# Kernel optimization log

Measured on AMD Instinct MI355X. Metric: run time of the kernel, lower is better.

Reference implementation:

```python
import jax, jax.numpy as jnp
import numpy as np

NEG = -1e30  # finite stand-in for -inf (grad-safe)


def _ctc_loss(logits, logit_length, labels):
    """CTC negative log-likelihood per example.

    logits: [B, T, V] (blank index 0), logit_length: [B] int,
    labels: [B, L] int padded with -1.
    """
    B, T, V = logits.shape
    L = labels.shape[1]
    S = 2 * L + 1  # extended label length (blanks interleaved)

    label_len = jnp.sum(labels >= 0, axis=1)          # [B]
    lab = jnp.where(labels < 0, 0, labels)            # pad -> blank for safe gathers
    ext = jnp.zeros((B, S), dtype=lab.dtype).at[:, 1::2].set(lab)  # [B, S]

    log_probs = jax.nn.log_softmax(logits, axis=-1)   # [B, T, V]
    # emission log-prob of each extended symbol at each time: [B, T, S]
    lp_ext = jnp.take_along_axis(log_probs, ext[:, None, :], axis=2)

    # skip (s-2) transition allowed only for non-blank symbols differing from s-2
    ext_m2 = jnp.pad(ext, ((0, 0), (2, 0)), constant_values=-1)[:, :S]
    allow_skip = (ext != 0) & (ext != ext_m2)         # [B, S]

    alpha0 = (jnp.full((B, S), NEG, dtype=logits.dtype)
              .at[:, 0].set(lp_ext[:, 0, 0])
              .at[:, 1].set(lp_ext[:, 0, 1]))

    def step(alpha, lp_t):  # alpha, lp_t: [B, S]
        a1 = jnp.pad(alpha, ((0, 0), (1, 0)), constant_values=NEG)[:, :S]
        a2 = jnp.pad(alpha, ((0, 0), (2, 0)), constant_values=NEG)[:, :S]
        a2 = jnp.where(allow_skip, a2, NEG)
        new = lp_t + jnp.logaddexp(jnp.logaddexp(alpha, a1), a2)
        return new, new

    lp_tm = jnp.moveaxis(lp_ext, 1, 0)                # [T, B, S] time-major
    _, alphas = jax.lax.scan(step, alpha0, lp_tm[1:])
    alphas = jnp.concatenate([alpha0[None], alphas], axis=0)  # [T, B, S]

    # read trellis at each example's final frame
    t_idx = jnp.clip(logit_length, 1, T) - 1          # [B]
    alpha_fin = alphas[t_idx, jnp.arange(B)]          # [B, S]
    s_last = 2 * label_len                            # final blank position
    a_blank = jnp.take_along_axis(alpha_fin, s_last[:, None], axis=1)[:, 0]
    a_label = jnp.take_along_axis(alpha_fin, jnp.maximum(s_last - 1, 0)[:, None], axis=1)[:, 0]
    return -jnp.logaddexp(a_blank, a_label)           # [B]


def setup_inputs() -> dict:
    key = jax.random.key(0)
    k1, k2, k3, k4 = jax.random.split(key, 4)
    B, T, V, L = 64, 1000, 64, 150
    logits = jax.random.normal(k1, (B, T, V), dtype=jnp.float32)
    # raw sample counts; min 100000 guarantees logit_length >= 2*L+1 (valid CTC)
    audio_length = jax.random.randint(k2, (B,), 100000, 256000, dtype=jnp.int32)
    label_vals = jax.random.randint(k3, (B, L), 1, V, dtype=jnp.int32)  # no blanks
    label_len = jax.random.randint(k4, (B,), 100, L + 1, dtype=jnp.int32)
    pos = jnp.arange(L)[None, :]
    labels = jnp.where(pos < label_len[:, None], label_vals, -1)
    return {"logits": logits, "audio_length": audio_length, "labels": labels}


def reference(logits, audio_length, labels):
    # length transform from train_step: ceil((len+1)/128), then truncating /2
    ll = jnp.ceil((audio_length.astype(jnp.float32) + 1.0) / 128.0).astype(jnp.int32)
    logit_length = ll // 2
    per_ex = _ctc_loss(logits, logit_length, labels)
    return jnp.mean(per_ex)
```

## Files before the change

kernel.cpp:

```cpp
#include <hip/hip_runtime.h>


#define VV 64
#define L2E 1.4426950408889634f
#define LN2D 0.6931471805599453
#define CH 8

__global__ __launch_bounds__(256) void lse_kernel(const float4* __restrict__ lg4,
                                                  const int* __restrict__ audio_len,
                                                  double* __restrict__ sumlse,
                                                  float* __restrict__ out,
                                                  int T) {
    if (blockIdx.x == 0 && blockIdx.y == 0 && threadIdx.x == 0) out[0] = 0.0f;
    const int b = blockIdx.y;
    const int tl = threadIdx.x >> 4;
    const int q = threadIdx.x & 15;
    const int t = blockIdx.x * 16 + tl;
    int al = audio_len[b];
    int Tb = ((al + 128) >> 7) >> 1;
    if (Tb < 1) Tb = 1;
    if (Tb > T) Tb = T;

    __shared__ double part[16];
    double v = 0.0;
    if (t < Tb) {
        float4 x = lg4[((size_t)b * T + t) * 16 + q];
        float m = fmaxf(fmaxf(x.x, x.y), fmaxf(x.z, x.w));
        #pragma unroll
        for (int off = 8; off >= 1; off >>= 1) m = fmaxf(m, __shfl_xor(m, off));
        float s = __expf(x.x - m) + __expf(x.y - m) + __expf(x.z - m) + __expf(x.w - m);
        #pragma unroll
        for (int off = 8; off >= 1; off >>= 1) s += __shfl_xor(s, off);
        v = (double)(m + __logf(s));
    }
    if (q == 0) part[tl] = v;
    __syncthreads();
    if (threadIdx.x == 0) {
        double s = 0.0;
        #pragma unroll
        for (int i = 0; i < 16; ++i) s += part[i];
        if (s != 0.0) atomicAdd(&sumlse[b], s);
    }
}


#define LOADM(E, TB, DIRSGN)                                                    \
    do {                                                                        \
        _Pragma("unroll")                                                       \
        for (int k_ = 0; k_ < CH; ++k_) {                                       \
            int tt_ = (TB) + (DIRSGN) * k_;                                     \
            if (tt_ < 0) tt_ = 0;                                               \
            if (tt_ > tf) tt_ = tf;                                             \
            const float* fr_ = lg + ((size_t)tt_ << 6);                         \
            _Pragma("unroll")                                                   \
            for (int i_ = 0; i_ < 5; ++i_) E[i_][k_] = fr_[sym[i_]];            \
        }                                                                       \
    } while (0)

#define CONV(E)                                                                 \
    do {                                                                        \
        _Pragma("unroll")                                                       \
        for (int i_ = 0; i_ < 5; ++i_) {                                        \
            _Pragma("unroll")                                                   \
            for (int k_ = 0; k_ < CH; ++k_)                                     \
                E[i_][k_] = __builtin_amdgcn_exp2f(E[i_][k_] * L2E);            \
        }                                                                       \
    } while (0)

#define PROCF(E, STEP0, MASKED)                                                 \
    do {                                                                        \
        _Pragma("unroll")                                                       \
        for (int k_ = 0; k_ < CH; ++k_) {                                       \
            double a_ = __shfl_up(p[4], 1);                                     \
            double b_ = __shfl_up(p[3], 1);                                     \
            if (lane == 0) { a_ = 0.0; b_ = 0.0; }                              \
            double e_[5];                                                       \
            _Pragma("unroll")                                                   \
            for (int i_ = 0; i_ < 5; ++i_) e_[i_] = (double)E[i_][k_];          \
            double n0_ = e_[0] * (p[0] + a_ + skd[0] * b_);                     \
            double n1_ = e_[1] * (p[1] + p[0] + skd[1] * a_);                   \
            double n2_ = e_[2] * (p[2] + p[1] + skd[2] * p[0]);                 \
            double n3_ = e_[3] * (p[3] + p[2] + skd[3] * p[1]);                 \
            double n4_ = e_[4] * (p[4] + p[3] + skd[4] * p[2]);                 \
            if (MASKED) {                                                       \
                bool act_ = ((STEP0) + k_) < nst_;                              \
                p[0] = act_ ? n0_ : p[0]; p[1] = act_ ? n1_ : p[1];             \
                p[2] = act_ ? n2_ : p[2]; p[3] = act_ ? n3_ : p[3];             \
                p[4] = act_ ? n4_ : p[4];                                       \
            } else {                                                            \
                p[0] = n0_; p[1] = n1_; p[2] = n2_; p[3] = n3_; p[4] = n4_;     \
            }                                                                   \
        }                                                                       \
    } while (0)

#define PROCB(E, STEP0, MASKED)                                                 \
    do {                                                                        \
        _Pragma("unroll")                                                       \
        for (int k_ = 0; k_ < CH; ++k_) {                                       \
               \
            double pn0_ = __shfl_down(p[0], 1);                                 \
            double pn1_ = __shfl_down(p[1], 1);                                 \
            float en0_ = __shfl_down(E[0][k_], 1);                              \
            float en1_ = __shfl_down(E[1][k_], 1);                              \
            if (lane == 63) { pn0_ = 0.0; pn1_ = 0.0; }                         \
            double u_[5];                                                       \
            _Pragma("unroll")                                                   \
            for (int i_ = 0; i_ < 5; ++i_) u_[i_] = p[i_] * (double)E[i_][k_];  \
            double u5_ = pn0_ * (double)en0_;                                   \
            double u6_ = pn1_ * (double)en1_;                                   \
            double n0_ = u_[0] + u_[1] + skd[2] * u_[2];                        \
            double n1_ = u_[1] + u_[2] + skd[3] * u_[3];                        \
            double n2_ = u_[2] + u_[3] + skd[4] * u_[4];                        \
            double n3_ = u_[3] + u_[4] + skd[5] * u5_;                          \
            double n4_ = u_[4] + u5_ + skd[6] * u6_;                            \
            if (MASKED) {                                                       \
                bool act_ = ((STEP0) + k_) < nst_;                              \
                p[0] = act_ ? n0_ : p[0]; p[1] = act_ ? n1_ : p[1];             \
                p[2] = act_ ? n2_ : p[2]; p[3] = act_ ? n3_ : p[3];             \
                p[4] = act_ ? n4_ : p[4];                                       \
            } else {                                                            \
                p[0] = n0_; p[1] = n1_; p[2] = n2_; p[3] = n3_; p[4] = n4_;     \
            }                                                                   \
        }                                                                       \
    } while (0)

#define RENORM()                                                                \
    do {                                                                        \
        double mx_ = fmax(fmax(fmax(p[0], p[1]), fmax(p[2], p[3])), p[4]);      \
        int ex_ = (__double2hiint(mx_) >> 20) & 0x7ff;                          \
        _Pragma("unroll")                                                       \
        for (int o_ = 32; o_ >= 1; o_ >>= 1) {                                  \
            int t_ = __shfl_xor(ex_, o_);                                       \
            ex_ = t_ > ex_ ? t_ : ex_;                                          \
        }                                                                       \
        if (ex_ > 0) {                                                          \
            Cexp += ex_ - 1023;                                                 \
            double r_ = __hiloint2double((2046 - ex_) << 20, 0);                \
            _Pragma("unroll")                                                   \
            for (int i_ = 0; i_ < 5; ++i_) p[i_] *= r_;                         \
        }                                                                       \
    } while (0)

__global__ __launch_bounds__(128, 1) void ctc_kernel(const float* __restrict__ lgall,
                                                     const int* __restrict__ audio_len,
                                                     const int* __restrict__ labels,
                                                     const double* __restrict__ sumlse,
                                                     float* __restrict__ out,
                                                     int B, int T, int L) {
    const int b = blockIdx.x;
    const int tid = threadIdx.x;
    const int lane = tid & 63;
    const int wid = tid >> 6;
    const int S = 2 * L + 1;
    const float* lg = lgall + (size_t)b * T * VV;

    int al = audio_len[b];
    int Tb = ((al + 128) >> 7) >> 1;
    if (Tb < 1) Tb = 1;
    if (Tb > T) Tb = T;
    const int tf = Tb - 1;
    const int mid = tf >> 1;

    __shared__ int lab_sh[152];
    __shared__ double beta_sh[324];
    __shared__ double sumlse_sh;
    __shared__ int cexpb_sh;

    for (int k = tid; k < L; k += 128) lab_sh[k] = labels[b * L + k];
    __syncthreads();

    int cnt = 0;
    for (int k = lane; k < L; k += 64) cnt += (lab_sh[k] >= 0) ? 1 : 0;
    #pragma unroll
    for (int off = 32; off >= 1; off >>= 1) cnt += __shfl_xor(cnt, off);
    const int s_last = 2 * cnt;

    int sym[5];
    double skd[7];
    #pragma unroll
    for (int i = 0; i < 7; ++i) {
        int s = lane * 5 + i;
        int sy = 0;
        double sk = 0.0;
        if (s < S && (s & 1)) {
            int lv = lab_sh[s >> 1];
            sy = lv < 0 ? 0 : lv;
            if (s >= 3 && sy != 0) {
                int lv2 = lab_sh[(s >> 1) - 1];
                int s2 = lv2 < 0 ? 0 : lv2;
                sk = (sy != s2) ? 1.0 : 0.0;
            }
        }
        if (i < 5) sym[i] = sy;
        skd[i] = sk;
    }

    double p[5];
    int Cexp = 0;

    if (wid == 0) {
        {
            #pragma unroll
            for (int i = 0; i < 5; ++i) {
                float x = lg[sym[i]];
                int s = lane * 5 + i;
                p[i] = (s <= 1) ? (double)__builtin_amdgcn_exp2f(x * L2E) : 0.0;
            }
        }
        const int nst_ = mid;
        if (nst_ > 0) {
            const int nch = (nst_ + CH - 1) / CH;
            float eA[5][CH], eB[5][CH];
            LOADM(eA, 1, +1);
            int base = 1, c = 0, step0 = 0;
            for (;;) {
                if (c + 1 < nch) LOADM(eB, base + CH, +1);
                CONV(eA);
                if (c == nch - 1) { PROCF(eA, step0, 1); break; }
                PROCF(eA, step0, 0);
                ++c; step0 += CH; base += CH;
                if ((c & 3) == 0) RENORM();
                if (c + 1 < nch) LOADM(eA, base + CH, +1);
                CONV(eB);
                if (c == nch - 1) { PROCF(eB, step0, 1); break; }
                PROCF(eB, step0, 0);
                ++c; step0 += CH; base += CH;
                if ((c & 3) == 0) RENORM();
            }
        }
        RENORM();
    } else {
        #pragma unroll
        for (int i = 0; i < 5; ++i) {
            int s = lane * 5 + i;
            p[i] = (s == s_last || s == s_last - 1) ? 1.0 : 0.0;
        }
        const int nst_ = tf - mid;
        if (nst_ > 0) {
            const int nch = (nst_ + CH - 1) / CH;
            float eA[5][CH], eB[5][CH];
            LOADM(eA, tf, -1);
            int base = tf, c = 0, step0 = 0;
            for (;;) {
                if (c + 1 < nch) LOADM(eB, base - CH, -1);
                CONV(eA);
                if (c == nch - 1) { PROCB(eA, step0, 1); break; }
                PROCB(eA, step0, 0);
                ++c; step0 += CH; base -= CH;
                if ((c & 3) == 0) RENORM();
                if (c + 1 < nch) LOADM(eA, base - CH, -1);
                CONV(eB);
                if (c == nch - 1) { PROCB(eB, step0, 1); break; }
                PROCB(eB, step0, 0);
                ++c; step0 += CH; base -= CH;
                if ((c & 3) == 0) RENORM();
            }
        }
        RENORM();
        #pragma unroll
        for (int i = 0; i < 5; ++i) beta_sh[lane * 5 + i] = p[i];
        if (lane == 0) { cexpb_sh = Cexp; sumlse_sh = sumlse[b]; }
    }
    __syncthreads();

    if (wid == 0) {
        double dot = 0.0;
        #pragma unroll
        for (int i = 0; i < 5; ++i) dot += p[i] * beta_sh[lane * 5 + i];
        #pragma unroll
        for (int o = 32; o >= 1; o >>= 1) dot += __shfl_xor(dot, o);
        if (lane == 0) {
            dot = fmax(dot, 1e-290);
            double lp = log(dot) + (double)(Cexp + cexpb_sh) * LN2D - sumlse_sh;
            atomicAdd(out, (float)(-lp / (double)B));
        }
    }
}

extern "C" void kernel_launch(void* const* d_in, const int* in_sizes, int n_in,
                              void* d_out, int out_size, void* d_ws, size_t ws_size,
                              hipStream_t stream) {
    const float* logits = (const float*)d_in[0];
    const int* audio = (const int*)d_in[1];
    const int* labels = (const int*)d_in[2];
    float* out = (float*)d_out;

    int B = in_sizes[1];
    int L = in_sizes[2] / B;
    int T = in_sizes[0] / (B * VV);

    double* sumlse = (double*)d_ws;
    hipMemsetAsync(sumlse, 0, (size_t)B * sizeof(double), stream);

    dim3 gA((T + 15) / 16, B);
    lse_kernel<<<gA, 256, 0, stream>>>((const float4*)logits, audio, sumlse, out, T);
    ctc_kernel<<<B, 128, 0, stream>>>(logits, audio, labels, sumlse, out, B, T, L);
}
```

Baseline: 169.8 us.

## Fuse log-sum-exp into CTC kernel via third wave and hand-scheduled loads

```diff
diff --git a/kernel.cpp b/kernel.cpp
--- a/kernel.cpp
+++ b/kernel.cpp
@@ -6,56 +6,44 @@
 #define LN2D 0.6931471805599453
 #define CH 8
 
-__global__ __launch_bounds__(256) void lse_kernel(const float4* __restrict__ lg4,
-                                                  const int* __restrict__ audio_len,
-                                                  double* __restrict__ sumlse,
-                                                  float* __restrict__ out,
-                                                  int T) {
-    if (blockIdx.x == 0 && blockIdx.y == 0 && threadIdx.x == 0) out[0] = 0.0f;
-    const int b = blockIdx.y;
-    const int tl = threadIdx.x >> 4;
-    const int q = threadIdx.x & 15;
-    const int t = blockIdx.x * 16 + tl;
-    int al = audio_len[b];
-    int Tb = ((al + 128) >> 7) >> 1;
-    if (Tb < 1) Tb = 1;
-    if (Tb > T) Tb = T;
-
-    __shared__ double part[16];
-    double v = 0.0;
-    if (t < Tb) {
-        float4 x = lg4[((size_t)b * T + t) * 16 + q];
-        float m = fmaxf(fmaxf(x.x, x.y), fmaxf(x.z, x.w));
-        #pragma unroll
-        for (int off = 8; off >= 1; off >>= 1) m = fmaxf(m, __shfl_xor(m, off));
-        float s = __expf(x.x - m) + __expf(x.y - m) + __expf(x.z - m) + __expf(x.w - m);
-        #pragma unroll
-        for (int off = 8; off >= 1; off >>= 1) s += __shfl_xor(s, off);
-        v = (double)(m + __logf(s));
-    }
-    if (q == 0) part[tl] = v;
-    __syncthreads();
-    if (threadIdx.x == 0) {
-        double s = 0.0;
-        #pragma unroll
-        for (int i = 0; i < 16; ++i) s += part[i];
-        if (s != 0.0) atomicAdd(&sumlse[b], s);
-    }
+template <int IMM>
+__device__ __forceinline__ float gload(const float* p) {
+    float r;
+    asm volatile("global_load_dword %0, %1, off offset:%2"
+                 : "=v"(r) : "v"(p), "n"(IMM));
+    return r;
 }
 
-
-#define LOADM(E, TB, DIRSGN)                                                    \
-    do {                                                                        \
-        _Pragma("unroll")                                                       \
-        for (int k_ = 0; k_ < CH; ++k_) {                                       \
-            int tt_ = (TB) + (DIRSGN) * k_;                                     \
-            if (tt_ < 0) tt_ = 0;                                               \
-            if (tt_ > tf) tt_ = tf;                                             \
-            const float* fr_ = lg + ((size_t)tt_ << 6);                         \
-            _Pragma("unroll")                                                   \
-            for (int i_ = 0; i_ < 5; ++i_) E[i_][k_] = fr_[sym[i_]];            \
-        }                                                                       \
-    } while (0)
+#define ISSUE5(E, K, IMM)                                                       \
+    do {                                                                        \
+        E[0][K] = gload<IMM>(ap0); E[1][K] = gload<IMM>(ap1);                   \
+        E[2][K] = gload<IMM>(ap2); E[3][K] = gload<IMM>(ap3);                   \
+        E[4][K] = gload<IMM>(ap4);                                              \
+    } while (0)
+
+#define ISSUEF(E)                                                               \
+    do { ISSUE5(E,0,0);    ISSUE5(E,1,256);  ISSUE5(E,2,512);  ISSUE5(E,3,768); \
+         ISSUE5(E,4,1024); ISSUE5(E,5,1280); ISSUE5(E,6,1536); ISSUE5(E,7,1792);} while (0)
+
+#define ISSUEB(E)                                                               \
+    do { ISSUE5(E,0,0);     ISSUE5(E,1,-256);  ISSUE5(E,2,-512);  ISSUE5(E,3,-768); \
+         ISSUE5(E,4,-1024); ISSUE5(E,5,-1280); ISSUE5(E,6,-1536); ISSUE5(E,7,-1792);} while (0)
+
+#define SETAPF(CB)                                                              \
+    do { int cb_ = (CB); if (cb_ > tf - 7) cb_ = tf - 7; if (cb_ < 0) cb_ = 0;  \
+         const float* fr_ = lg + ((size_t)cb_ << 6);                            \
+         ap0 = fr_ + sym[0]; ap1 = fr_ + sym[1]; ap2 = fr_ + sym[2];            \
+         ap3 = fr_ + sym[3]; ap4 = fr_ + sym[4]; } while (0)
+
+#define SETAPB(CB)                                                              \
+    do { int cb_ = (CB); if (cb_ < 7) cb_ = 7; if (cb_ > tf) cb_ = tf;          \
+         const float* fr_ = lg + ((size_t)cb_ << 6);                            \
+         ap0 = fr_ + sym[0]; ap1 = fr_ + sym[1]; ap2 = fr_ + sym[2];            \
+         ap3 = fr_ + sym[3]; ap4 = fr_ + sym[4]; } while (0)
+
+#define WAITCNT                                                                 \
+    do { asm volatile("s_waitcnt vmcnt(40)" ::: "memory");                      \
+         __builtin_amdgcn_sched_barrier(0); } while (0)
 
 #define CONV(E)                                                                 \
     do {                                                                        \
@@ -97,7 +85,6 @@
     do {                                                                        \
         _Pragma("unroll")                                                       \
         for (int k_ = 0; k_ < CH; ++k_) {                                       \
-               \
             double pn0_ = __shfl_down(p[0], 1);                                 \
             double pn1_ = __shfl_down(p[1], 1);                                 \
             float en0_ = __shfl_down(E[0][k_], 1);                              \
@@ -141,10 +128,9 @@
         }                                                                       \
     } while (0)
 
-__global__ __launch_bounds__(128, 1) void ctc_kernel(const float* __restrict__ lgall,
+__global__ __launch_bounds__(192, 1) void ctc_kernel(const float* __restrict__ lgall,
                                                      const int* __restrict__ audio_len,
                                                      const int* __restrict__ labels,
-                                                     const double* __restrict__ sumlse,
                                                      float* __restrict__ out,
                                                      int B, int T, int L) {
     const int b = blockIdx.x;
@@ -166,7 +152,7 @@
     __shared__ double sumlse_sh;
     __shared__ int cexpb_sh;
 
-    for (int k = tid; k < L; k += 128) lab_sh[k] = labels[b * L + k];
+    for (int k = tid; k < L; k += 192) lab_sh[k] = labels[b * L + k];
     __syncthreads();
 
     int cnt = 0;
@@ -199,37 +185,37 @@
     int Cexp = 0;
 
     if (wid == 0) {
-        {
-            #pragma unroll
-            for (int i = 0; i < 5; ++i) {
-                float x = lg[sym[i]];
-                int s = lane * 5 + i;
-                p[i] = (s <= 1) ? (double)__builtin_amdgcn_exp2f(x * L2E) : 0.0;
-            }
+        #pragma unroll
+        for (int i = 0; i < 5; ++i) {
+            float x = lg[sym[i]];
+            int s = lane * 5 + i;
+            p[i] = (s <= 1) ? (double)__builtin_amdgcn_exp2f(x * L2E) : 0.0;
         }
         const int nst_ = mid;
         if (nst_ > 0) {
             const int nch = (nst_ + CH - 1) / CH;
             float eA[5][CH], eB[5][CH];
-            LOADM(eA, 1, +1);
-            int base = 1, c = 0, step0 = 0;
+            const float *ap0, *ap1, *ap2, *ap3, *ap4;
+            SETAPF(1);      ISSUEF(eA);
+            SETAPF(1 + CH); ISSUEF(eB);
+            int c = 0, step0 = 0, cbn = 1 + 2 * CH;
             for (;;) {
-                if (c + 1 < nch) LOADM(eB, base + CH, +1);
-                CONV(eA);
+                WAITCNT; CONV(eA);
                 if (c == nch - 1) { PROCF(eA, step0, 1); break; }
                 PROCF(eA, step0, 0);
-                ++c; step0 += CH; base += CH;
+                SETAPF(cbn); ISSUEF(eA); cbn += CH;
+                ++c; step0 += CH;
                 if ((c & 3) == 0) RENORM();
-                if (c + 1 < nch) LOADM(eA, base + CH, +1);
-                CONV(eB);
+                WAITCNT; CONV(eB);
                 if (c == nch - 1) { PROCF(eB, step0, 1); break; }
                 PROCF(eB, step0, 0);
-                ++c; step0 += CH; base += CH;
+                SETAPF(cbn); ISSUEF(eB); cbn += CH;
+                ++c; step0 += CH;
                 if ((c & 3) == 0) RENORM();
             }
         }
         RENORM();
-    } else {
+    } else if (wid == 1) {
         #pragma unroll
         for (int i = 0; i < 5; ++i) {
             int s = lane * 5 + i;
@@ -239,27 +225,52 @@
         if (nst_ > 0) {
             const int nch = (nst_ + CH - 1) / CH;
             float eA[5][CH], eB[5][CH];
-            LOADM(eA, tf, -1);
-            int base = tf, c = 0, step0 = 0;
+            const float *ap0, *ap1, *ap2, *ap3, *ap4;
+            SETAPB(tf);      ISSUEB(eA);
+            SETAPB(tf - CH); ISSUEB(eB);
+            int c = 0, step0 = 0, cbn = tf - 2 * CH;
             for (;;) {
-                if (c + 1 < nch) LOADM(eB, base - CH, -1);
-                CONV(eA);
+                WAITCNT; CONV(eA);
                 if (c == nch - 1) { PROCB(eA, step0, 1); break; }
                 PROCB(eA, step0, 0);
-                ++c; step0 += CH; base -= CH;
+                SETAPB(cbn); ISSUEB(eA); cbn -= CH;
+                ++c; step0 += CH;
                 if ((c & 3) == 0) RENORM();
-                if (c + 1 < nch) LOADM(eA, base - CH, -1);
-                CONV(eB);
+                WAITCNT; CONV(eB);
                 if (c == nch - 1) { PROCB(eB, step0, 1); break; }
                 PROCB(eB, step0, 0);
-                ++c; step0 += CH; base -= CH;
+                SETAPB(cbn); ISSUEB(eB); cbn -= CH;
+                ++c; step0 += CH;
                 if ((c & 3) == 0) RENORM();
             }
         }
         RENORM();
         #pragma unroll
         for (int i = 0; i < 5; ++i) beta_sh[lane * 5 + i] = p[i];
-        if (lane == 0) { cexpb_sh = Cexp; sumlse_sh = sumlse[b]; }
+        if (lane == 0) cexpb_sh = Cexp;
+    } else {
+        const float4* lg4 = (const float4*)lg;
+        const int q = lane & 15;
+        const int fg = lane >> 4;
+        double acc = 0.0;
+        for (int g0 = 0; g0 * 4 < Tb; ++g0) {
+            int t = g0 * 4 + fg;
+            double v = 0.0;
+            if (t < Tb) {
+                float4 x = lg4[t * 16 + q];
+                float m = fmaxf(fmaxf(x.x, x.y), fmaxf(x.z, x.w));
+                #pragma unroll
+                for (int off = 8; off >= 1; off >>= 1) m = fmaxf(m, __shfl_xor(m, off));
+                float s = __expf(x.x - m) + __expf(x.y - m) + __expf(x.z - m) + __expf(x.w - m);
+                #pragma unroll
+                for (int off = 8; off >= 1; off >>= 1) s += __shfl_xor(s, off);
+                v = (double)(m + __logf(s));
+            }
+            if (q == 0) acc += v;
+        }
+        #pragma unroll
+        for (int o = 32; o >= 1; o >>= 1) acc += __shfl_xor(acc, o);
+        if (lane == 0) sumlse_sh = acc;
     }
     __syncthreads();
 
@@ -289,10 +300,6 @@
     int L = in_sizes[2] / B;
     int T = in_sizes[0] / (B * VV);
 
-    double* sumlse = (double*)d_ws;
-    hipMemsetAsync(sumlse, 0, (size_t)B * sizeof(double), stream);
-
-    dim3 gA((T + 15) / 16, B);
-    lse_kernel<<<gA, 256, 0, stream>>>((const float4*)logits, audio, sumlse, out, T);
-    ctc_kernel<<<B, 128, 0, stream>>>(logits, audio, labels, sumlse, out, B, T, L);
+    hipMemsetAsync(out, 0, sizeof(float), stream);
+    ctc_kernel<<<B, 192, 0, stream>>>(logits, audio, labels, out, B, T, L);
 }
```

New measurement: 202.5 us. +19.2%, slower.
